# Kernel tuning notes

Measured on AMD Instinct MI355X. Metric: run time of the kernel, lower is better.

## Reference

```python
import jax, jax.numpy as jnp
import numpy as np

N_LAYERS = 4
D_MODEL = 256
N_HEADS = 8
D_FF = 2 * D_MODEL
EPS_ATTN = 1e-6
EPS_LN = 1e-5


def setup_inputs() -> dict:
    key = jax.random.key(0)
    ks = jax.random.split(key, 20)
    C, F, L = D_MODEL, D_FF, N_LAYERS
    s = 0.02
    return {
        "ref_feature": jax.random.normal(ks[0], (4, C, 128, 128), jnp.float32),
        # per-layer stacked params (torch nn.Linear convention: y = x @ W.T + b)
        "Wq": jax.random.normal(ks[1], (L, C, C), jnp.float32) * s,
        "bq": jnp.zeros((L, C), jnp.float32),
        "Wk": jax.random.normal(ks[2], (L, C, C), jnp.float32) * s,
        "bk": jnp.zeros((L, C), jnp.float32),
        "Wv": jax.random.normal(ks[3], (L, C, C), jnp.float32) * s,
        "bv": jnp.zeros((L, C), jnp.float32),
        "Wo": jax.random.normal(ks[4], (L, C, C), jnp.float32) * s,
        "bo": jnp.zeros((L, C), jnp.float32),
        "g1": jnp.ones((L, C), jnp.float32),
        "be1": jnp.zeros((L, C), jnp.float32),
        "W1": jax.random.normal(ks[5], (L, F, C), jnp.float32) * s,
        "c1": jnp.zeros((L, F), jnp.float32),
        "W2": jax.random.normal(ks[6], (L, C, F), jnp.float32) * s,
        "c2": jnp.zeros((L, C), jnp.float32),
        "g2": jnp.ones((L, C), jnp.float32),
        "be2": jnp.zeros((L, C), jnp.float32),
    }


def _layer_norm(x, g, b):
    m = jnp.mean(x, axis=-1, keepdims=True)
    v = jnp.mean(jnp.square(x - m), axis=-1, keepdims=True)
    return (x - m) * jax.lax.rsqrt(v + EPS_LN) * g + b


def _feature_map(x):
    return jax.nn.elu(x) + 1.0


def reference(ref_feature, Wq, bq, Wk, bk, Wv, bv, Wo, bo,
              g1, be1, W1, c1, W2, c2, g2, be2):
    N, C, H, W = ref_feature.shape
    Hh, D = N_HEADS, C // N_HEADS
    # patch embed: flatten to tokens [N, HW, C]
    x = ref_feature.reshape(N, C, H * W).transpose(0, 2, 1)

    def body(x, p):
        (Wq_, bq_, Wk_, bk_, Wv_, bv_, Wo_, bo_,
         g1_, be1_, W1_, c1_, W2_, c2_, g2_, be2_) = p
        L = x.shape[1]
        q = (x @ Wq_.T + bq_).reshape(N, L, Hh, D)
        k = (x @ Wk_.T + bk_).reshape(N, L, Hh, D)
        v = (x @ Wv_.T + bv_).reshape(N, L, Hh, D)
        Q = _feature_map(q)
        K = _feature_map(k)
        KV = jnp.einsum('nshd,nshm->nhmd', K, v)            # [N,H,D,D]
        Z = 1.0 / (jnp.einsum('nlhd,nhd->nlh', Q, K.sum(axis=1)) + EPS_ATTN)
        attn = jnp.einsum('nlhd,nhmd,nlh->nlhm', Q, KV, Z).reshape(N, L, C)
        x = _layer_norm(x + attn @ Wo_.T + bo_, g1_, be1_)
        y = jax.nn.relu(x @ W1_.T + c1_) @ W2_.T + c2_
        x = _layer_norm(x + y, g2_, be2_)
        return x, x

    params = (Wq, bq, Wk, bk, Wv, bv, Wo, bo,
              g1, be1, W1, c1, W2, c2, g2, be2)
    _, ys = jax.lax.scan(body, x, params)
    # ys: [n_layers, N, HW, C] -> [n_layers, N, C, H, W]
    return ys.transpose(0, 1, 3, 2).reshape(N_LAYERS, N, C, H, W)
```

## Files before the change

### kernel.cpp

```cpp
#include <hip/hip_runtime.h>
#include <hip/hip_bf16.h>
#include <math.h>

#define NB     4
#define CDIM   256
#define HWDIM  16384
#define LTOK   16384
#define NH     8
#define HD     32
#define FF     512
#define MTOK   (NB * LTOK)
#define NLAYER 4

typedef __bf16 bf16x8 __attribute__((ext_vector_type(8)));
typedef __bf16 bf16x4 __attribute__((ext_vector_type(4)));
typedef float  floatx4 __attribute__((ext_vector_type(4)));

#define GLD16(gp, lp)                                                        \
    __builtin_amdgcn_global_load_lds(                                        \
        (const __attribute__((address_space(1))) void*)(gp),                 \
        (__attribute__((address_space(3))) void*)(lp), 16, 0, 0)

__global__ __launch_bounds__(256)
void f2b_kernel(const float* __restrict__ in, __bf16* __restrict__ out)
{
    int i = (blockIdx.x * 256 + threadIdx.x) * 4;
    float4 f = *(const float4*)&in[i];
    bf16x4 h;
    h[0] = (__bf16)f.x; h[1] = (__bf16)f.y; h[2] = (__bf16)f.z; h[3] = (__bf16)f.w;
    *(bf16x4*)&out[i] = h;
}

__global__ __launch_bounds__(256)
void patch_embed(const float* __restrict__ in, __bf16* __restrict__ out)
{
    __shared__ float tile[32][33];
    const int n = blockIdx.z;
    const int hw0 = blockIdx.x * 32, c0 = blockIdx.y * 32;
    const int tx = threadIdx.x, ty = threadIdx.y;
#pragma unroll
    for (int i = 0; i < 32; i += 8)
        tile[ty + i][tx] = in[(long long)n * CDIM * HWDIM + (long long)(c0 + ty + i) * HWDIM + hw0 + tx];
    __syncthreads();
#pragma unroll
    for (int i = 0; i < 32; i += 8)
        out[(long long)(n * HWDIM + hw0 + ty + i) * CDIM + c0 + tx] = (__bf16)tile[tx][ty + i];
}

__global__ __launch_bounds__(256)
void out_transpose(const __bf16* __restrict__ X, float* __restrict__ out)
{
    __shared__ float tile[32][33];
    const int n = blockIdx.z;
    const int c0 = blockIdx.x * 32, l0 = blockIdx.y * 32;
    const int tx = threadIdx.x, ty = threadIdx.y;
#pragma unroll
    for (int i = 0; i < 32; i += 8)
        tile[ty + i][tx] = (float)X[(long long)(n * LTOK + l0 + ty + i) * CDIM + c0 + tx];
    __syncthreads();
#pragma unroll
    for (int i = 0; i < 32; i += 8)
        out[(long long)n * CDIM * LTOK + (long long)(c0 + ty + i) * LTOK + l0 + tx] = tile[tx][ty + i];
}

template <int ACT>
__global__ __launch_bounds__(256)
void gemm_bf16(const __bf16* __restrict__ A, const __bf16* __restrict__ B,
               const float* __restrict__ bias, __bf16* __restrict__ C,
               int M, int K, int O)
{
    __shared__ __bf16 Asl[128 * 64];
    __shared__ __bf16 Bsl[128 * 64];

    const int tid  = threadIdx.x;
    const int lane = tid & 63;
    const int wave = tid >> 6;
    const int m0   = blockIdx.x * 128;
    const int n0   = blockIdx.y * 128;
    const int l15  = lane & 15;
    const int quad = lane >> 4;
    const int wm   = (wave & 1) * 64;
    const int wn   = (wave >> 1) * 64;

    floatx4 acc[4][4];
#pragma unroll
    for (int i = 0; i < 4; ++i)
#pragma unroll
        for (int j = 0; j < 4; ++j)
            acc[i][j] = (floatx4){0.f, 0.f, 0.f, 0.f};

    for (int k0 = 0; k0 < K; k0 += 64) {
        __syncthreads();
#pragma unroll
        for (int i = 0; i < 4; ++i) {
            int s   = wave * 256 + i * 64 + lane;
            int row = s >> 3, kq = s & 7;
            GLD16(&A[(long long)(m0 + row) * K + k0 + kq * 8],
                  &Asl[(wave * 256 + i * 64) * 8]);
        }
#pragma unroll
        for (int i = 0; i < 4; ++i) {
            int s   = wave * 256 + i * 64 + lane;
            int row = s >> 3, kq = s & 7;
            GLD16(&B[(long long)(n0 + row) * K + k0 + kq * 8],
                  &Bsl[(wave * 256 + i * 64) * 8]);
        }
        __syncthreads();

#pragma unroll
        for (int ko = 0; ko < 2; ++ko) {
            bf16x8 af[4], bfr[4];
#pragma unroll
            for (int mt = 0; mt < 4; ++mt)
                af[mt] = *(const bf16x8*)&Asl[(wm + mt * 16 + l15) * 64 + ko * 32 + quad * 8];
#pragma unroll
            for (int nt = 0; nt < 4; ++nt)
                bfr[nt] = *(const bf16x8*)&Bsl[(wn + nt * 16 + l15) * 64 + ko * 32 + quad * 8];
#pragma unroll
            for (int mt = 0; mt < 4; ++mt)
#pragma unroll
                for (int nt = 0; nt < 4; ++nt)
                    acc[mt][nt] = __builtin_amdgcn_mfma_f32_16x16x32_bf16(
                        af[mt], bfr[nt], acc[mt][nt], 0, 0, 0);
        }
    }

#pragma unroll
    for (int mt = 0; mt < 4; ++mt) {
#pragma unroll
        for (int nt = 0; nt < 4; ++nt) {
            int col  = n0 + wn + nt * 16 + l15;
            float bv = bias[col];
            int rowb = m0 + wm + mt * 16 + quad * 4;
#pragma unroll
            for (int r = 0; r < 4; ++r) {
                float v = acc[mt][nt][r] + bv;
                if (ACT == 1) v = v > 0.f ? v + 1.f : __expf(v);
                if (ACT == 2) v = v > 0.f ? v : 0.f;
                C[(long long)(rowb + r) * O + col] = (__bf16)v;
            }
        }
    }
}

__global__ __launch_bounds__(256)
void kv_kernel(const __bf16* __restrict__ Kg, const __bf16* __restrict__ Vg,
               float* __restrict__ KV, float* __restrict__ KS)
{
    __shared__ float Ks[64 * 32];
    __shared__ float Vs[64 * 32];
    const int n = blockIdx.z, h = blockIdx.y;
    const int tid = threadIdx.x;
    const int d  = tid & 31;
    const int m4 = tid >> 5;

    float acc[4] = {0.f, 0.f, 0.f, 0.f};
    float ksum = 0.f;

    for (int sub = 0; sub < 8; ++sub) {
        int s0 = blockIdx.x * 512 + sub * 64;
        __syncthreads();
        {
            int e   = tid * 8;
            int tok = e >> 5, dd = e & 31;
            long long gi = (long long)(n * LTOK + s0 + tok) * CDIM + h * HD + dd;
            bf16x8 kk = *(const bf16x8*)&Kg[gi];
            bf16x8 vv = *(const bf16x8*)&Vg[gi];
#pragma unroll
            for (int j = 0; j < 8; ++j) {
                Ks[e + j] = (float)kk[j];
                Vs[e + j] = (float)vv[j];
            }
        }
        __syncthreads();
#pragma unroll 4
        for (int s = 0; s < 64; ++s) {
            float kd = Ks[s * 32 + d];
            if (m4 == 0) ksum += kd;
#pragma unroll
            for (int j = 0; j < 4; ++j)
                acc[j] += Vs[s * 32 + m4 * 4 + j] * kd;
        }
    }
#pragma unroll
    for (int j = 0; j < 4; ++j)
        atomicAdd(&KV[(((n * NH + h) * HD) + (m4 * 4 + j)) * HD + d], acc[j]);
    if (m4 == 0)
        atomicAdd(&KS[(n * NH + h) * HD + d], ksum);
}

__global__ __launch_bounds__(256)
void attn_kernel(const __bf16* __restrict__ Q, const float* __restrict__ KV,
                 const float* __restrict__ KS, __bf16* __restrict__ out)
{
    __shared__ float kv_lds[NH * 32 * 33];
    __shared__ float ks_lds[NH * 32];
    __shared__ float q_lds[16 * 256];

    const int n = blockIdx.y;
    const int tid = threadIdx.x;
    const int h = tid >> 5;
    const int m = tid & 31;

    for (int i = tid; i < NH * 32 * 32; i += 256) {
        int hh  = i >> 10;
        int rem = i & 1023;
        int mm  = rem >> 5;
        int dd  = rem & 31;
        kv_lds[hh * 1056 + mm * 33 + dd] = KV[n * (NH * 32 * 32) + i];
    }
    ks_lds[tid] = KS[n * (NH * 32) + tid];
    __syncthreads();

    for (int it = 0; it < 4; ++it) {
        int l0 = blockIdx.x * 64 + it * 16;
#pragma unroll
        for (int i = 0; i < 4; ++i) {
            int e = tid * 4 + i * 1024;
            int row = e >> 8, col = e & 255;
            bf16x4 q4 = *(const bf16x4*)&Q[(long long)(n * LTOK + l0 + row) * CDIM + col];
            float4 f;
            f.x = (float)q4[0]; f.y = (float)q4[1]; f.z = (float)q4[2]; f.w = (float)q4[3];
            *(float4*)&q_lds[e] = f;
        }
        __syncthreads();
        for (int t = 0; t < 16; ++t) {
            const float* qr  = &q_lds[t * 256 + h * 32];
            const float* kvr = &kv_lds[h * 1056 + m * 33];
            const float* ksr = &ks_lds[h * 32];
            float den = 0.f, num = 0.f;
#pragma unroll
            for (int d = 0; d < 32; ++d) {
                float qd = qr[d];
                den += qd * ksr[d];
                num += qd * kvr[d];
            }
            out[(long long)(n * LTOK + l0 + t) * CDIM + tid] = (__bf16)(num / (den + 1e-6f));
        }
        __syncthreads();
    }
}

__global__ __launch_bounds__(256)
void ln_kernel(__bf16* __restrict__ X, const __bf16* __restrict__ T,
               const float* __restrict__ g, const float* __restrict__ b)
{
    const int tid  = threadIdx.x;
    const int wave = tid >> 6;
    const int lane = tid & 63;
    const long long tok = (long long)blockIdx.x * 4 + wave;
    const long long base = tok * CDIM + lane * 4;

    bf16x4 xv = *(const bf16x4*)&X[base];
    bf16x4 tv = *(const bf16x4*)&T[base];
    float v[4];
#pragma unroll
    for (int j = 0; j < 4; ++j) v[j] = (float)xv[j] + (float)tv[j];

    float s = v[0] + v[1] + v[2] + v[3];
#pragma unroll
    for (int off = 32; off > 0; off >>= 1) s += __shfl_xor(s, off, 64);
    float mean = s * (1.f / 256.f);

    float dv[4];
    float ss = 0.f;
#pragma unroll
    for (int j = 0; j < 4; ++j) { dv[j] = v[j] - mean; ss += dv[j] * dv[j]; }
#pragma unroll
    for (int off = 32; off > 0; off >>= 1) ss += __shfl_xor(ss, off, 64);
    float rstd = rsqrtf(ss * (1.f / 256.f) + 1e-5f);

    const float4 gv = ((const float4*)g)[lane];
    const float4 bv = ((const float4*)b)[lane];
    bf16x4 o;
    o[0] = (__bf16)(dv[0] * rstd * gv.x + bv.x);
    o[1] = (__bf16)(dv[1] * rstd * gv.y + bv.y);
    o[2] = (__bf16)(dv[2] * rstd * gv.z + bv.z);
    o[3] = (__bf16)(dv[3] * rstd * gv.w + bv.w);
    *(bf16x4*)&X[base] = o;
}

extern "C" void kernel_launch(void* const* d_in, const int* in_sizes, int n_in,
                              void* d_out, int out_size, void* d_ws, size_t ws_size,
                              hipStream_t stream)
{
    const float* ref = (const float*)d_in[0];
    const float* Wq  = (const float*)d_in[1];  const float* bq = (const float*)d_in[2];
    const float* Wk  = (const float*)d_in[3];  const float* bk = (const float*)d_in[4];
    const float* Wv  = (const float*)d_in[5];  const float* bv = (const float*)d_in[6];
    const float* Wo  = (const float*)d_in[7];  const float* bo = (const float*)d_in[8];
    const float* g1  = (const float*)d_in[9];  const float* be1 = (const float*)d_in[10];
    const float* W1  = (const float*)d_in[11]; const float* c1 = (const float*)d_in[12];
    const float* W2  = (const float*)d_in[13]; const float* c2 = (const float*)d_in[14];
    const float* g2  = (const float*)d_in[15]; const float* be2 = (const float*)d_in[16];
    float* out = (float*)d_out;

    const size_t SZ = (size_t)MTOK * CDIM;
    __bf16* Xb = (__bf16*)d_ws;
    __bf16* Qb = Xb + SZ;
    __bf16* Kb = Qb + SZ;
    __bf16* Vb = Kb + SZ;
    __bf16* Hb = Vb + SZ;
    float*  KVb = (float*)(Hb + 2 * SZ);
    float*  KSb = KVb + NB * NH * HD * HD;
    __bf16* Wqb = (__bf16*)(KSb + NB * NH * HD);
    const size_t WC = (size_t)NLAYER * CDIM * CDIM;
    const size_t WF = (size_t)NLAYER * FF * CDIM;
    __bf16* Wkb = Wqb + WC;
    __bf16* Wvb = Wkb + WC;
    __bf16* Wob = Wvb + WC;
    __bf16* W1b = Wob + WC;
    __bf16* W2b = W1b + WF;

    f2b_kernel<<<WC / 1024, 256, 0, stream>>>(Wq, Wqb);
    f2b_kernel<<<WC / 1024, 256, 0, stream>>>(Wk, Wkb);
    f2b_kernel<<<WC / 1024, 256, 0, stream>>>(Wv, Wvb);
    f2b_kernel<<<WC / 1024, 256, 0, stream>>>(Wo, Wob);
    f2b_kernel<<<WF / 1024, 256, 0, stream>>>(W1, W1b);
    f2b_kernel<<<WF / 1024, 256, 0, stream>>>(W2, W2b);

    dim3 tb(32, 8);
    patch_embed<<<dim3(HWDIM / 32, CDIM / 32, NB), tb, 0, stream>>>(ref, Xb);

    for (int l = 0; l < NLAYER; ++l) {
        const __bf16* Wq_l = Wqb + (size_t)l * CDIM * CDIM;
        const __bf16* Wk_l = Wkb + (size_t)l * CDIM * CDIM;
        const __bf16* Wv_l = Wvb + (size_t)l * CDIM * CDIM;
        const __bf16* Wo_l = Wob + (size_t)l * CDIM * CDIM;
        const __bf16* W1_l = W1b + (size_t)l * FF * CDIM;
        const __bf16* W2_l = W2b + (size_t)l * CDIM * FF;
        const float* bq_l = bq + (size_t)l * CDIM;
        const float* bk_l = bk + (size_t)l * CDIM;
        const float* bv_l = bv + (size_t)l * CDIM;
        const float* bo_l = bo + (size_t)l * CDIM;
        const float* c1_l = c1 + (size_t)l * FF;
        const float* c2_l = c2 + (size_t)l * CDIM;
        const float* g1_l = g1 + (size_t)l * CDIM;
        const float* g2_l = g2 + (size_t)l * CDIM;
        const float* be1_l = be1 + (size_t)l * CDIM;
        const float* be2_l = be2 + (size_t)l * CDIM;

        dim3 gC(MTOK / 128, CDIM / 128);
        dim3 gF(MTOK / 128, FF / 128);

        gemm_bf16<1><<<gC, 256, 0, stream>>>(Xb, Wq_l, bq_l, Qb, MTOK, CDIM, CDIM);
        gemm_bf16<1><<<gC, 256, 0, stream>>>(Xb, Wk_l, bk_l, Kb, MTOK, CDIM, CDIM);
        gemm_bf16<0><<<gC, 256, 0, stream>>>(Xb, Wv_l, bv_l, Vb, MTOK, CDIM, CDIM);

        hipMemsetAsync(KVb, 0, (NB * NH * HD * HD + NB * NH * HD) * sizeof(float), stream);
        kv_kernel<<<dim3(LTOK / 512, NH, NB), 256, 0, stream>>>(Kb, Vb, KVb, KSb);

        attn_kernel<<<dim3(LTOK / 64, NB), 256, 0, stream>>>(Qb, KVb, KSb, Kb);
        gemm_bf16<0><<<gC, 256, 0, stream>>>(Kb, Wo_l, bo_l, Vb, MTOK, CDIM, CDIM);

        ln_kernel<<<MTOK / 4, 256, 0, stream>>>(Xb, Vb, g1_l, be1_l);

        gemm_bf16<2><<<gF, 256, 0, stream>>>(Xb, W1_l, c1_l, Hb, MTOK, CDIM, FF);
        gemm_bf16<0><<<gC, 256, 0, stream>>>(Hb, W2_l, c2_l, Vb, MTOK, FF, CDIM);

        ln_kernel<<<MTOK / 4, 256, 0, stream>>>(Xb, Vb, g2_l, be2_l);

        out_transpose<<<dim3(CDIM / 32, LTOK / 32, NB), tb, 0, stream>>>(
            Xb, out + (size_t)l * NB * CDIM * LTOK);
    }
}
```

Measured before the change: 1.693 ms.

## Fuse QKV GEMMs, vectorize GEMM epilogue, register-cache KV in attention, vectorize transpose

The three Q/K/V projection GEMMs become one launch whose y-grid selects the weight, bias and output. The GEMM swaps MFMA operand order so each lane holds four consecutive columns, letting the epilogue use vector bias loads and 8-byte bf16x4 stores. The attention kernel keeps its per-thread KV row and K-sum in registers instead of LDS, and the output transpose uses vector loads and float4 stores with a 1D block. These cut launch overhead and narrow memory accesses, at the cost of more registers in the attention kernel.

Measured after the change: 1.657 ms. 2.1% less time.

```diff
diff --git a/kernel.cpp b/kernel.cpp
--- a/kernel.cpp
+++ b/kernel.cpp
@@ -53,15 +53,61 @@
     __shared__ float tile[32][33];
     const int n = blockIdx.z;
     const int c0 = blockIdx.x * 32, l0 = blockIdx.y * 32;
-    const int tx = threadIdx.x, ty = threadIdx.y;
-#pragma unroll
-    for (int i = 0; i < 32; i += 8)
-        tile[ty + i][tx] = (float)X[(long long)(n * LTOK + l0 + ty + i) * CDIM + c0 + tx];
+    const int tid = threadIdx.x;
+    {
+        int row = tid >> 3, cq = tid & 7;
+        bf16x4 x4 = *(const bf16x4*)&X[(long long)(n * LTOK + l0 + row) * CDIM + c0 + cq * 4];
+#pragma unroll
+        for (int j = 0; j < 4; ++j)
+            tile[row][cq * 4 + j] = (float)x4[j];
+    }
     __syncthreads();
-#pragma unroll
-    for (int i = 0; i < 32; i += 8)
-        out[(long long)n * CDIM * LTOK + (long long)(c0 + ty + i) * LTOK + l0 + tx] = tile[tx][ty + i];
-}
+    {
+        int r = tid >> 3, lg = tid & 7;
+        float4 o;
+        o.x = tile[lg * 4 + 0][r];
+        o.y = tile[lg * 4 + 1][r];
+        o.z = tile[lg * 4 + 2][r];
+        o.w = tile[lg * 4 + 3][r];
+        *(float4*)&out[(long long)n * CDIM * LTOK + (long long)(c0 + r) * LTOK + l0 + lg * 4] = o;
+    }
+}
+
+#define GEMM_STAGE(Aq, Bq, Kdim)                                             \
+    __syncthreads();                                                         \
+    _Pragma("unroll")                                                        \
+    for (int i = 0; i < 4; ++i) {                                            \
+        int s = wave * 256 + i * 64 + lane;                                  \
+        int row = s >> 3, kq = s & 7;                                        \
+        GLD16(&(Aq)[(long long)(m0 + row) * (Kdim) + k0 + kq * 8],           \
+              &Asl[(wave * 256 + i * 64) * 8]);                              \
+    }                                                                        \
+    _Pragma("unroll")                                                        \
+    for (int i = 0; i < 4; ++i) {                                            \
+        int s = wave * 256 + i * 64 + lane;                                  \
+        int row = s >> 3, kq = s & 7;                                        \
+        GLD16(&(Bq)[(long long)(n0 + row) * (Kdim) + k0 + kq * 8],           \
+              &Bsl[(wave * 256 + i * 64) * 8]);                              \
+    }                                                                        \
+    __syncthreads();
+
+#define GEMM_MFMA()                                                          \
+    _Pragma("unroll")                                                        \
+    for (int ko = 0; ko < 2; ++ko) {                                         \
+        bf16x8 af[4], bfr[4];                                                \
+        _Pragma("unroll")                                                    \
+        for (int mt = 0; mt < 4; ++mt)                                       \
+            af[mt] = *(const bf16x8*)&Asl[(wm + mt * 16 + l15) * 64 + ko * 32 + quad * 8]; \
+        _Pragma("unroll")                                                    \
+        for (int nt = 0; nt < 4; ++nt)                                       \
+            bfr[nt] = *(const bf16x8*)&Bsl[(wn + nt * 16 + l15) * 64 + ko * 32 + quad * 8]; \
+        _Pragma("unroll")                                                    \
+        for (int mt = 0; mt < 4; ++mt)                                       \
+            _Pragma("unroll")                                                \
+            for (int nt = 0; nt < 4; ++nt)                                   \
+                acc[mt][nt] = __builtin_amdgcn_mfma_f32_16x16x32_bf16(       \
+                    bfr[nt], af[mt], acc[mt][nt], 0, 0, 0);                  \
+    }
 
 template <int ACT>
 __global__ __launch_bounds__(256)
@@ -90,55 +136,85 @@
             acc[i][j] = (floatx4){0.f, 0.f, 0.f, 0.f};
 
     for (int k0 = 0; k0 < K; k0 += 64) {
-        __syncthreads();
-#pragma unroll
-        for (int i = 0; i < 4; ++i) {
-            int s   = wave * 256 + i * 64 + lane;
-            int row = s >> 3, kq = s & 7;
-            GLD16(&A[(long long)(m0 + row) * K + k0 + kq * 8],
-                  &Asl[(wave * 256 + i * 64) * 8]);
-        }
-#pragma unroll
-        for (int i = 0; i < 4; ++i) {
-            int s   = wave * 256 + i * 64 + lane;
-            int row = s >> 3, kq = s & 7;
-            GLD16(&B[(long long)(n0 + row) * K + k0 + kq * 8],
-                  &Bsl[(wave * 256 + i * 64) * 8]);
-        }
-        __syncthreads();
-
-#pragma unroll
-        for (int ko = 0; ko < 2; ++ko) {
-            bf16x8 af[4], bfr[4];
-#pragma unroll
-            for (int mt = 0; mt < 4; ++mt)
-                af[mt] = *(const bf16x8*)&Asl[(wm + mt * 16 + l15) * 64 + ko * 32 + quad * 8];
-#pragma unroll
-            for (int nt = 0; nt < 4; ++nt)
-                bfr[nt] = *(const bf16x8*)&Bsl[(wn + nt * 16 + l15) * 64 + ko * 32 + quad * 8];
-#pragma unroll
-            for (int mt = 0; mt < 4; ++mt)
-#pragma unroll
-                for (int nt = 0; nt < 4; ++nt)
-                    acc[mt][nt] = __builtin_amdgcn_mfma_f32_16x16x32_bf16(
-                        af[mt], bfr[nt], acc[mt][nt], 0, 0, 0);
-        }
+        GEMM_STAGE(A, B, K)
+        GEMM_MFMA()
     }
 
 #pragma unroll
     for (int mt = 0; mt < 4; ++mt) {
+        int row = m0 + wm + mt * 16 + l15;
 #pragma unroll
         for (int nt = 0; nt < 4; ++nt) {
-            int col  = n0 + wn + nt * 16 + l15;
-            float bv = bias[col];
-            int rowb = m0 + wm + mt * 16 + quad * 4;
+            int col0 = n0 + wn + nt * 16 + quad * 4;
+            float4 bb = *(const float4*)&bias[col0];
+            bf16x4 o;
 #pragma unroll
             for (int r = 0; r < 4; ++r) {
-                float v = acc[mt][nt][r] + bv;
+                float v = acc[mt][nt][r] + ((r == 0) ? bb.x : (r == 1) ? bb.y : (r == 2) ? bb.z : bb.w);
                 if (ACT == 1) v = v > 0.f ? v + 1.f : __expf(v);
                 if (ACT == 2) v = v > 0.f ? v : 0.f;
-                C[(long long)(rowb + r) * O + col] = (__bf16)v;
+                o[r] = (__bf16)v;
             }
+            *(bf16x4*)&C[(long long)row * O + col0] = o;
+        }
+    }
+}
+
+__global__ __launch_bounds__(256)
+void gemm_qkv(const __bf16* __restrict__ X,
+              const __bf16* __restrict__ Wq, const __bf16* __restrict__ Wk,
+              const __bf16* __restrict__ Wv,
+              const float* __restrict__ bq, const float* __restrict__ bk,
+              const float* __restrict__ bv,
+              __bf16* __restrict__ Qo, __bf16* __restrict__ Ko,
+              __bf16* __restrict__ Vo)
+{
+    __shared__ __bf16 Asl[128 * 64];
+    __shared__ __bf16 Bsl[128 * 64];
+
+    const int sel = blockIdx.y >> 1;
+    const __bf16* B    = (sel == 0) ? Wq : (sel == 1) ? Wk : Wv;
+    const float*  bias = (sel == 0) ? bq : (sel == 1) ? bk : bv;
+    __bf16*       C    = (sel == 0) ? Qo : (sel == 1) ? Ko : Vo;
+    const bool do_elu  = sel < 2;
+
+    const int tid  = threadIdx.x;
+    const int lane = tid & 63;
+    const int wave = tid >> 6;
+    const int m0   = blockIdx.x * 128;
+    const int n0   = (blockIdx.y & 1) * 128;
+    const int l15  = lane & 15;
+    const int quad = lane >> 4;
+    const int wm   = (wave & 1) * 64;
+    const int wn   = (wave >> 1) * 64;
+
+    floatx4 acc[4][4];
+#pragma unroll
+    for (int i = 0; i < 4; ++i)
+#pragma unroll
+        for (int j = 0; j < 4; ++j)
+            acc[i][j] = (floatx4){0.f, 0.f, 0.f, 0.f};
+
+    for (int k0 = 0; k0 < CDIM; k0 += 64) {
+        GEMM_STAGE(X, B, CDIM)
+        GEMM_MFMA()
+    }
+
+#pragma unroll
+    for (int mt = 0; mt < 4; ++mt) {
+        int row = m0 + wm + mt * 16 + l15;
+#pragma unroll
+        for (int nt = 0; nt < 4; ++nt) {
+            int col0 = n0 + wn + nt * 16 + quad * 4;
+            float4 bb = *(const float4*)&bias[col0];
+            bf16x4 o;
+#pragma unroll
+            for (int r = 0; r < 4; ++r) {
+                float v = acc[mt][nt][r] + ((r == 0) ? bb.x : (r == 1) ? bb.y : (r == 2) ? bb.z : bb.w);
+                if (do_elu) v = v > 0.f ? v + 1.f : __expf(v);
+                o[r] = (__bf16)v;
+            }
+            *(bf16x4*)&C[(long long)row * CDIM + col0] = o;
         }
     }
 }
@@ -193,27 +269,23 @@
 void attn_kernel(const __bf16* __restrict__ Q, const float* __restrict__ KV,
                  const float* __restrict__ KS, __bf16* __restrict__ out)
 {
-    __shared__ float kv_lds[NH * 32 * 33];
-    __shared__ float ks_lds[NH * 32];
     __shared__ float q_lds[16 * 256];
-
     const int n = blockIdx.y;
     const int tid = threadIdx.x;
     const int h = tid >> 5;
     const int m = tid & 31;
 
-    for (int i = tid; i < NH * 32 * 32; i += 256) {
-        int hh  = i >> 10;
-        int rem = i & 1023;
-        int mm  = rem >> 5;
-        int dd  = rem & 31;
-        kv_lds[hh * 1056 + mm * 33 + dd] = KV[n * (NH * 32 * 32) + i];
-    }
-    ks_lds[tid] = KS[n * (NH * 32) + tid];
-    __syncthreads();
+    float4 kvr[8], ksr[8];
+    {
+        const float4* kvp = (const float4*)&KV[(((long long)n * NH + h) * HD + m) * HD];
+        const float4* ksp = (const float4*)&KS[((long long)n * NH + h) * HD];
+#pragma unroll
+        for (int i = 0; i < 8; ++i) { kvr[i] = kvp[i]; ksr[i] = ksp[i]; }
+    }
 
     for (int it = 0; it < 4; ++it) {
         int l0 = blockIdx.x * 64 + it * 16;
+        __syncthreads();
 #pragma unroll
         for (int i = 0; i < 4; ++i) {
             int e = tid * 4 + i * 1024;
@@ -224,20 +296,18 @@
             *(float4*)&q_lds[e] = f;
         }
         __syncthreads();
+#pragma unroll 2
         for (int t = 0; t < 16; ++t) {
-            const float* qr  = &q_lds[t * 256 + h * 32];
-            const float* kvr = &kv_lds[h * 1056 + m * 33];
-            const float* ksr = &ks_lds[h * 32];
-            float den = 0.f, num = 0.f;
-#pragma unroll
-            for (int d = 0; d < 32; ++d) {
-                float qd = qr[d];
-                den += qd * ksr[d];
-                num += qd * kvr[d];
+            const float4* qr = (const float4*)&q_lds[t * 256 + h * 32];
+            float num = 0.f, den = 0.f;
+#pragma unroll
+            for (int i = 0; i < 8; ++i) {
+                float4 q4 = qr[i];
+                num += q4.x * kvr[i].x + q4.y * kvr[i].y + q4.z * kvr[i].z + q4.w * kvr[i].w;
+                den += q4.x * ksr[i].x + q4.y * ksr[i].y + q4.z * ksr[i].z + q4.w * ksr[i].w;
             }
             out[(long long)(n * LTOK + l0 + t) * CDIM + tid] = (__bf16)(num / (den + 1e-6f));
         }
-        __syncthreads();
     }
 }
 
@@ -343,9 +413,8 @@
         dim3 gC(MTOK / 128, CDIM / 128);
         dim3 gF(MTOK / 128, FF / 128);
 
-        gemm_bf16<1><<<gC, 256, 0, stream>>>(Xb, Wq_l, bq_l, Qb, MTOK, CDIM, CDIM);
-        gemm_bf16<1><<<gC, 256, 0, stream>>>(Xb, Wk_l, bk_l, Kb, MTOK, CDIM, CDIM);
-        gemm_bf16<0><<<gC, 256, 0, stream>>>(Xb, Wv_l, bv_l, Vb, MTOK, CDIM, CDIM);
+        gemm_qkv<<<dim3(MTOK / 128, 6), 256, 0, stream>>>(
+            Xb, Wq_l, Wk_l, Wv_l, bq_l, bk_l, bv_l, Qb, Kb, Vb);
 
         hipMemsetAsync(KVb, 0, (NB * NH * HD * HD + NB * NH * HD) * sizeof(float), stream);
         kv_kernel<<<dim3(LTOK / 512, NH, NB), 256, 0, stream>>>(Kb, Vb, KVb, KSb);
@@ -360,7 +429,7 @@
 
         ln_kernel<<<MTOK / 4, 256, 0, stream>>>(Xb, Vb, g2_l, be2_l);
 
-        out_transpose<<<dim3(CDIM / 32, LTOK / 32, NB), tb, 0, stream>>>(
+        out_transpose<<<dim3(CDIM / 32, LTOK / 32, NB), 256, 0, stream>>>(
             Xb, out + (size_t)l * NB * CDIM * LTOK);
     }
 }
```
